# Kernel optimization log

Hardware: AMD Instinct MI355X
Metric: run time of the kernel (lower is better)

## Reference

```python
import jax, jax.numpy as jnp
import numpy as np

N2 = 128      # time horizon (days)
M = 16384     # number of regions / batched chains
START = 6     # seeding window (days with externally seeded cases)


def setup_inputs() -> dict:
    key = jax.random.key(0)
    k0, k1, k2, k3, k4 = jax.random.split(key, 5)
    # reproduction numbers R_t in [0, 2)
    rt = jax.random.uniform(k0, (N2, M), dtype=jnp.float32) * 2.0
    deaths_gt = jax.random.uniform(k1, (N2, M), dtype=jnp.float32)
    # serial-interval distribution (positive, sums to 1 so the recurrence stays bounded)
    si_raw = jax.random.uniform(k2, (N2,), dtype=jnp.float32)
    SI = si_raw / jnp.sum(si_raw)
    f_raw = jax.random.uniform(k3, (N2, M), dtype=jnp.float32)
    f = f_raw / jnp.sum(f_raw, axis=0, keepdims=True) * 0.01
    # seeded cases for the first START days
    seed = jax.random.uniform(k4, (START, M), dtype=jnp.float32)
    return {"rt": rt, "deaths_gt": deaths_gt, "SI": SI, "f": f,
            "seed": seed, "start": START}


def _predict_cases(rt, SI, seed, start):
    # prediction[i, m] = rt[i, m] * sum_{j < i} prediction[j, m] * SI[i - j]
    # sequential triangular recurrence over time -> lax.scan with full carry.
    n2, m = rt.shape
    idx = jnp.arange(n2)
    pred0 = jnp.zeros((n2, m), rt.dtype).at[:start].set(seed)

    def step(pred, i):
        d = i - idx                                   # SI lag for each j
        w = jnp.where(d > 0, SI[jnp.clip(d, 0, n2 - 1)], 0.0)  # [N2], zero for j >= i
        conv = w @ pred                               # [M]
        row = jnp.where(i >= start, rt[i] * conv, pred[i])
        return pred.at[i].set(row), None

    pred, _ = jax.lax.scan(step, pred0, jnp.arange(n2))
    return pred


def _predict_deaths(pred, f, start):
    # E_deaths[i, m] = sum_{j <= i-2} pred[j, m] * f[i-j, m]
    # = causal per-region convolution with lags d = i-j >= 2 (so zero f[0], f[1]).
    n2, m = pred.shape
    f_eff = f.at[:2].set(0.0)
    conv = jax.vmap(lambda p, k: jnp.convolve(p, k)[:n2],
                    in_axes=1, out_axes=1)(pred, f_eff)   # [N2, M]
    i = jnp.arange(n2)[:, None]
    # rows before `start` are untouched by the loop (0), row 0 is set to 1e-9
    return jnp.where(i >= start, conv, jnp.where(i == 0, 1e-9, 0.0))


def reference(rt, deaths_gt, SI, f, seed, start):
    cases_pred = _predict_cases(rt, SI, seed, start)
    deaths_pred = _predict_deaths(cases_pred, f, start)
    return jnp.mean((deaths_pred - deaths_gt) ** 2)  # nn.MSELoss
```

## Files before the change

### kernel.cpp

```cpp
#include <hip/hip_runtime.h>

#define N2 128
#define MM 16384
#define START 6
#define CB 32
#define BT 256
#define FSTR 143

__global__ __launch_bounds__(BT, 2) void npi_fused(
    const float* __restrict__ rt, const float* __restrict__ dgt,
    const float* __restrict__ si, const float* __restrict__ f,
    const float* __restrict__ seed, float* __restrict__ out)
{
    __shared__ float fC[CB * FSTR];
    __shared__ float hrow[16 * CB];
    __shared__ float si_s[N2];
    __shared__ float lred[4];

    const int t = threadIdx.x;
    const int c = t & 31;
    const int g = t >> 5;
    const int w = t >> 6;
    const int m = blockIdx.x * CB + c;

    float fregs[16];
#pragma unroll
    for (int q = 0; q < 16; ++q)
        fregs[q] = f[((g << 4) + q) * MM + m];
    float sd[START];
#pragma unroll
    for (int k = 0; k < START; ++k) sd[k] = seed[k * MM + m];
    float rtv[16];
#pragma unroll
    for (int k = 0; k < 16; ++k) rtv[k] = rt[k * MM + m];
    float dgv[2][8];
#pragma unroll
    for (int pass = 0; pass < 2; ++pass) {
        const int gi = pass ? (15 - g) : g;
#pragma unroll
        for (int r = 0; r < 8; ++r)
            dgv[pass][r] = dgt[((gi << 3) + r) * MM + m];
    }

    if (t < N2) si_s[t] = si[t];
#pragma unroll
    for (int z = 0; z < 2; ++z) {
        int p = t + z * BT;
        if (p < 15 * CB) fC[(p & 31) * FSTR + (p >> 5)] = 0.f;
    }
#pragma unroll
    for (int q = 0; q < 16; ++q) {
        int d = (g << 4) + q;
        fC[c * FSTR + 15 + d] = (d < 2) ? 0.f : fregs[q];
    }
    __syncthreads();

    float sr[16];
#pragma unroll
    for (int k = 1; k < 16; ++k) sr[k] = si_s[k];

    float Hacc[2][8], Eacc[2][8];
#pragma unroll
    for (int pass = 0; pass < 2; ++pass)
#pragma unroll
        for (int r = 0; r < 8; ++r) { Hacc[pass][r] = 0.f; Eacc[pass][r] = 0.f; }

    float v[16], rtn[16];

    {
        float p_[16];
#pragma unroll
        for (int k = 0; k < 16; ++k) p_[k] = 0.f;
#pragma unroll
        for (int k = 0; k < 16; ++k) {
            float vk;
            if (k < START) vk = sd[k];
            else vk = rtv[k] * (p_[k] + sr[1] * v[k - 1]);
            v[k] = vk;
#pragma unroll
            for (int k2 = k + 2; k2 < 16; ++k2)
                p_[k2] += sr[k2 - k] * vk;
        }
    }
#pragma unroll
    for (int k = 0; k < 16; ++k) rtn[k] = rt[(16 + k) * MM + m];
#pragma unroll
    for (int pass = 0; pass < 2; ++pass) {
        const int gi = pass ? (15 - g) : g;
        if (gi >= 2) {
            const int off = (gi << 3) - 15;
            float sw[23];
#pragma unroll
            for (int e = 0; e < 23; ++e) sw[e] = si_s[off + e];
#pragma unroll
            for (int r = 0; r < 8; ++r)
#pragma unroll
                for (int k = 0; k < 16; ++k)
                    Hacc[pass][r] += v[k] * sw[15 + r - k];
        }
        {
            const int offE = (gi << 3);
            float fw[23];
#pragma unroll
            for (int e = 0; e < 23; ++e) fw[e] = fC[c * FSTR + offE + e];
#pragma unroll
            for (int r = 0; r < 8; ++r)
#pragma unroll
                for (int k = 0; k < 16; ++k)
                    Eacc[pass][r] += v[k] * fw[15 + r - k];
        }
    }
#pragma unroll
    for (int k = 0; k < 16; ++k) rtv[k] = rtn[k];
    __syncthreads();

    for (int cb = 1; cb < 8; ++cb) {
#pragma unroll
        for (int pass = 0; pass < 2; ++pass) {
            const int gi = pass ? (15 - g) : g;
            if ((gi >> 1) == cb) {
#pragma unroll
                for (int r = 0; r < 8; ++r)
                    hrow[((((gi & 1) << 3) + r) << 5) + c] = Hacc[pass][r];
            }
        }
        __syncthreads();

        float p_[16];
#pragma unroll
        for (int k = 0; k < 16; ++k) p_[k] = hrow[(k << 5) + c];
#pragma unroll
        for (int k = 0; k < 16; ++k) {
            float vk = (k == 0) ? (rtv[0] * p_[0])
                                : (rtv[k] * (p_[k] + sr[1] * v[k - 1]));
            v[k] = vk;
#pragma unroll
            for (int k2 = k + 2; k2 < 16; ++k2)
                p_[k2] += sr[k2 - k] * vk;
        }
        if (cb < 7) {
#pragma unroll
            for (int k = 0; k < 16; ++k)
                rtn[k] = rt[(((cb + 1) << 4) + k) * MM + m];
        }

#pragma unroll
        for (int pass = 0; pass < 2; ++pass) {
            const int gi = pass ? (15 - g) : g;
            if (gi >= 2 * cb + 2) {
                const int off = (gi << 3) - (cb << 4) - 15;
                float sw[23];
#pragma unroll
                for (int e = 0; e < 23; ++e) sw[e] = si_s[off + e];
#pragma unroll
                for (int r = 0; r < 8; ++r)
#pragma unroll
                    for (int k = 0; k < 16; ++k)
                        Hacc[pass][r] += v[k] * sw[15 + r - k];
            }
            if (gi >= 2 * cb) {
                const int offE = (gi << 3) - (cb << 4);
                float fw[23];
#pragma unroll
                for (int e = 0; e < 23; ++e) fw[e] = fC[c * FSTR + offE + e];
#pragma unroll
                for (int r = 0; r < 8; ++r)
#pragma unroll
                    for (int k = 0; k < 16; ++k)
                        Eacc[pass][r] += v[k] * fw[15 + r - k];
            }
        }
#pragma unroll
        for (int k = 0; k < 16; ++k) rtv[k] = rtn[k];
        __syncthreads();
    }

    float lsum = 0.f;
#pragma unroll
    for (int pass = 0; pass < 2; ++pass) {
        const int gi = pass ? (15 - g) : g;
#pragma unroll
        for (int r = 0; r < 8; ++r) {
            const int i = (gi << 3) + r;
            float e = Eacc[pass][r];
            if (i == 0) e = 1e-9f;
            else if (i < START) e = 0.f;
            float diff = e - dgv[pass][r];
            lsum += diff * diff;
        }
    }
#pragma unroll
    for (int off = 32; off > 0; off >>= 1)
        lsum += __shfl_down(lsum, off, 64);
    if ((t & 63) == 0) lred[w] = lsum;
    __syncthreads();
    if (t == 0)
        atomicAdd(out, (lred[0] + lred[1] + lred[2] + lred[3]) *
                       (1.0f / ((float)N2 * (float)MM)));
}

extern "C" void kernel_launch(void* const* d_in, const int* in_sizes, int n_in,
                              void* d_out, int out_size, void* d_ws, size_t ws_size,
                              hipStream_t stream) {
    const float* rt   = (const float*)d_in[0];
    const float* dgt  = (const float*)d_in[1];
    const float* si   = (const float*)d_in[2];
    const float* f    = (const float*)d_in[3];
    const float* seed = (const float*)d_in[4];

    hipMemsetAsync(d_out, 0, sizeof(float), stream);
    npi_fused<<<dim3(MM / CB), dim3(BT), 0, stream>>>(
        rt, dgt, si, f, seed, (float*)d_out);
}
```

Baseline: 96.79 us.

## Double-buffer hrow, vectorize LDS window loads, drop extra barrier, defer dgt loads

Reads the SI and f windows from LDS with float4 loads, using a shifted SI array and padded strides so the reads stay aligned. The per-column hrow exchange becomes double-buffered with a per-thread row layout and vectorized writes and reads, which lets one __syncthreads per time block be removed. Ground-truth deaths are loaded at the end instead of being held in registers, lowering register pressure at the cost of global loads on the tail.

```diff
diff --git a/kernel.cpp b/kernel.cpp
--- a/kernel.cpp
+++ b/kernel.cpp
@@ -5,16 +5,27 @@
 #define START 6
 #define CB 32
 #define BT 256
-#define FSTR 143
+#define FSTR 148
+#define HSTR 20
+
+__device__ __forceinline__ void ldwin24(float* dst, const float* base) {
+    const float4* p4 = reinterpret_cast<const float4*>(base);
+#pragma unroll
+    for (int e = 0; e < 6; ++e) {
+        float4 q = p4[e];
+        dst[4 * e + 0] = q.x; dst[4 * e + 1] = q.y;
+        dst[4 * e + 2] = q.z; dst[4 * e + 3] = q.w;
+    }
+}
 
 __global__ __launch_bounds__(BT, 2) void npi_fused(
     const float* __restrict__ rt, const float* __restrict__ dgt,
     const float* __restrict__ si, const float* __restrict__ f,
     const float* __restrict__ seed, float* __restrict__ out)
 {
-    __shared__ float fC[CB * FSTR];
-    __shared__ float hrow[16 * CB];
-    __shared__ float si_s[N2];
+    __shared__ __align__(16) float fC[CB * FSTR];
+    __shared__ __align__(16) float hrow2[2 * CB * HSTR];
+    __shared__ __align__(16) float si_sh[128];
     __shared__ float lred[4];
 
     const int t = threadIdx.x;
@@ -33,16 +44,9 @@
     float rtv[16];
 #pragma unroll
     for (int k = 0; k < 16; ++k) rtv[k] = rt[k * MM + m];
-    float dgv[2][8];
-#pragma unroll
-    for (int pass = 0; pass < 2; ++pass) {
-        const int gi = pass ? (15 - g) : g;
-#pragma unroll
-        for (int r = 0; r < 8; ++r)
-            dgv[pass][r] = dgt[((gi << 3) + r) * MM + m];
-    }
-
-    if (t < N2) si_s[t] = si[t];
+
+    if (t < 127) si_sh[t] = si[t + 1];
+    if (t == 127) si_sh[127] = 0.f;
 #pragma unroll
     for (int z = 0; z < 2; ++z) {
         int p = t + z * BT;
@@ -57,7 +61,7 @@
 
     float sr[16];
 #pragma unroll
-    for (int k = 1; k < 16; ++k) sr[k] = si_s[k];
+    for (int k = 1; k < 16; ++k) sr[k] = si_sh[k - 1];
 
     float Hacc[2][8], Eacc[2][8];
 #pragma unroll
@@ -88,10 +92,8 @@
     for (int pass = 0; pass < 2; ++pass) {
         const int gi = pass ? (15 - g) : g;
         if (gi >= 2) {
-            const int off = (gi << 3) - 15;
-            float sw[23];
-#pragma unroll
-            for (int e = 0; e < 23; ++e) sw[e] = si_s[off + e];
+            float sw[24];
+            ldwin24(sw, &si_sh[(gi << 3) - 16]);
 #pragma unroll
             for (int r = 0; r < 8; ++r)
 #pragma unroll
@@ -99,10 +101,8 @@
                     Hacc[pass][r] += v[k] * sw[15 + r - k];
         }
         {
-            const int offE = (gi << 3);
-            float fw[23];
-#pragma unroll
-            for (int e = 0; e < 23; ++e) fw[e] = fC[c * FSTR + offE + e];
+            float fw[24];
+            ldwin24(fw, &fC[c * FSTR + (gi << 3)]);
 #pragma unroll
             for (int r = 0; r < 8; ++r)
 #pragma unroll
@@ -112,23 +112,30 @@
     }
 #pragma unroll
     for (int k = 0; k < 16; ++k) rtv[k] = rtn[k];
-    __syncthreads();
 
     for (int cb = 1; cb < 8; ++cb) {
+        float* hbuf = &hrow2[(cb & 1) * (CB * HSTR)];
 #pragma unroll
         for (int pass = 0; pass < 2; ++pass) {
             const int gi = pass ? (15 - g) : g;
             if ((gi >> 1) == cb) {
-#pragma unroll
-                for (int r = 0; r < 8; ++r)
-                    hrow[((((gi & 1) << 3) + r) << 5) + c] = Hacc[pass][r];
+                float4* hp = reinterpret_cast<float4*>(&hbuf[c * HSTR + ((gi & 1) << 3)]);
+                hp[0] = make_float4(Hacc[pass][0], Hacc[pass][1], Hacc[pass][2], Hacc[pass][3]);
+                hp[1] = make_float4(Hacc[pass][4], Hacc[pass][5], Hacc[pass][6], Hacc[pass][7]);
             }
         }
         __syncthreads();
 
         float p_[16];
-#pragma unroll
-        for (int k = 0; k < 16; ++k) p_[k] = hrow[(k << 5) + c];
+        {
+            const float4* pp = reinterpret_cast<const float4*>(&hbuf[c * HSTR]);
+#pragma unroll
+            for (int e = 0; e < 4; ++e) {
+                float4 q = pp[e];
+                p_[4 * e + 0] = q.x; p_[4 * e + 1] = q.y;
+                p_[4 * e + 2] = q.z; p_[4 * e + 3] = q.w;
+            }
+        }
 #pragma unroll
         for (int k = 0; k < 16; ++k) {
             float vk = (k == 0) ? (rtv[0] * p_[0])
@@ -148,10 +155,8 @@
         for (int pass = 0; pass < 2; ++pass) {
             const int gi = pass ? (15 - g) : g;
             if (gi >= 2 * cb + 2) {
-                const int off = (gi << 3) - (cb << 4) - 15;
-                float sw[23];
-#pragma unroll
-                for (int e = 0; e < 23; ++e) sw[e] = si_s[off + e];
+                float sw[24];
+                ldwin24(sw, &si_sh[(gi << 3) - (cb << 4) - 16]);
 #pragma unroll
                 for (int r = 0; r < 8; ++r)
 #pragma unroll
@@ -159,10 +164,8 @@
                         Hacc[pass][r] += v[k] * sw[15 + r - k];
             }
             if (gi >= 2 * cb) {
-                const int offE = (gi << 3) - (cb << 4);
-                float fw[23];
-#pragma unroll
-                for (int e = 0; e < 23; ++e) fw[e] = fC[c * FSTR + offE + e];
+                float fw[24];
+                ldwin24(fw, &fC[c * FSTR + (gi << 3) - (cb << 4)]);
 #pragma unroll
                 for (int r = 0; r < 8; ++r)
 #pragma unroll
@@ -172,7 +175,6 @@
         }
 #pragma unroll
         for (int k = 0; k < 16; ++k) rtv[k] = rtn[k];
-        __syncthreads();
     }
 
     float lsum = 0.f;
@@ -185,7 +187,7 @@
             float e = Eacc[pass][r];
             if (i == 0) e = 1e-9f;
             else if (i < START) e = 0.f;
-            float diff = e - dgv[pass][r];
+            float diff = e - dgt[i * MM + m];
             lsum += diff * diff;
         }
     }
```

After: 98.16 us. No clear change (+1.4%).
